# Performance work log

Hardware: AMD Instinct MI355X
Metric: run time of the kernel (lower is better)

The kernel has to match this reference:

```python
import jax, jax.numpy as jnp
import numpy as np

N, E, IN, H, O = 50000, 800000, 256, 8, 32


def setup_inputs() -> dict:
    key = jax.random.key(0)
    ks = jax.random.split(key, 8)
    feat = jax.random.normal(ks[0], (N, IN), dtype=jnp.float32)
    src = jax.random.randint(ks[1], (E,), 0, N, dtype=jnp.int32)
    dst = jax.random.randint(ks[2], (E,), 0, N, dtype=jnp.int32)
    # Xavier-normal-ish parameter init
    W = jax.random.normal(ks[3], (IN, H * O), dtype=jnp.float32) * (2.0 / (IN + H * O)) ** 0.5
    attn_l = jax.random.normal(ks[4], (H, O), dtype=jnp.float32) * (2.0 / (1 + H * O)) ** 0.5
    attn_r = jax.random.normal(ks[5], (H, O), dtype=jnp.float32) * (2.0 / (1 + H * O)) ** 0.5
    bias = jnp.zeros((H * O,), dtype=jnp.float32)
    return {"feat": feat, "W": W, "attn_l": attn_l, "attn_r": attn_r, "bias": bias, "src": src, "dst": dst}


def reference(feat, W, attn_l, attn_r, bias, src, dst):
    # Linear projection: [N, IN] @ [IN, H*O] -> [N, H, O]
    ft = (feat @ W).reshape(-1, H, O)
    # Additive attention logits per node, per head
    el = jnp.einsum('nho,ho->nh', ft, attn_l)  # [N, H]
    er = jnp.einsum('nho,ho->nh', ft, attn_r)  # [N, H]
    # Edge-wise: e = leaky_relu(el[u] + er[v])
    e = jax.nn.leaky_relu(el[src] + er[dst], negative_slope=0.2)  # [E, H]
    # Segment softmax over incoming edges of each destination node
    emax = jax.ops.segment_max(e, dst, num_segments=N)            # [N, H]
    ee = jnp.exp(e - emax[dst])                                   # [E, H]
    denom = jax.ops.segment_sum(ee, dst, num_segments=N)          # [N, H]
    a = ee / denom[dst]                                           # [E, H]
    # Weighted scatter-sum aggregation: sum_u a_{uv} * ft_u
    msg = ft[src] * a[:, :, None]                                 # [E, H, O]
    rst = jax.ops.segment_sum(msg, dst, num_segments=N)           # [N, H, O]
    rst = rst + bias.reshape(1, H, O)
    return rst
```

## Files before the change

### kernel.cpp

```cpp
#include <hip/hip_runtime.h>

#define N_NODES 50000
#define N_EDGES 800000
#define NPAD    50176
#define SPILL_CAP 8192
#define GEMM_BLOCKS 782
#define BUCKET_BLOCKS 1563

typedef __bf16 bf16x8 __attribute__((ext_vector_type(8)));
typedef float  fx4    __attribute__((ext_vector_type(4)));
typedef unsigned short us4 __attribute__((ext_vector_type(4)));
typedef unsigned short us8 __attribute__((ext_vector_type(8)));

__device__ __forceinline__ float b2f(unsigned short u) {
    return __uint_as_float(((unsigned)u) << 16);
}
__device__ __forceinline__ unsigned short f2b(float f) {
    unsigned x = __float_as_uint(f);
    return (unsigned short)((x + 0x7FFFu + ((x >> 16) & 1u)) >> 16);
}

__global__ __launch_bounds__(256) void prep_w(
    const float* __restrict__ W,
    const float* __restrict__ attn_l, const float* __restrict__ attn_r,
    unsigned short* __restrict__ Wt,
    unsigned short* __restrict__ M2t_hi, unsigned short* __restrict__ M2t_lo,
    int* __restrict__ cursor, int* __restrict__ spill_n) {
    int b = blockIdx.x, k = threadIdx.x;
    if (b < 256) {
        Wt[b * 256 + k] = f2b(W[k * 256 + b]);
    } else if (b < 272) {
        int j = b - 256;
        const float* av = (j < 8) ? (attn_l + j * 32) : (attn_r + (j - 8) * 32);
        int c0 = (j & 7) * 32;
        float s = 0.f;
#pragma unroll
        for (int o = 0; o < 32; ++o) s += W[k * 256 + c0 + o] * av[o];
        unsigned short h = f2b(s);
        M2t_hi[j * 256 + k] = h;
        M2t_lo[j * 256 + k] = f2b(s - b2f(h));
    } else {
        cursor[(b - 272) * 256 + k] = 0;
        if (b == 272 && k == 0) *spill_n = 0;
    }
}

__global__ __launch_bounds__(512) void gemm_bucket(
    const float* __restrict__ feat,
    const unsigned short* __restrict__ Wt,
    const unsigned short* __restrict__ M2t_hi,
    const unsigned short* __restrict__ M2t_lo,
    unsigned short* __restrict__ ft,
    float* __restrict__ el, float* __restrict__ er,
    const int* __restrict__ src, const int* __restrict__ dst,
    int* __restrict__ cursor, unsigned short* __restrict__ inedge,
    int* __restrict__ spill_n, int2* __restrict__ spill, int stride) {
    __shared__ unsigned short Alds[64 * 264];

    if (blockIdx.x >= GEMM_BLOCKS) {
        int t = (blockIdx.x - GEMM_BLOCKS) * 512 + threadIdx.x;
        if (t < N_EDGES) {
            int s = src[t], d = dst[t];
            int idx = atomicAdd(&cursor[d], 1);
            if (idx < stride) {
                inedge[(size_t)d * stride + idx] = (unsigned short)s;
            } else {
                int sp = atomicAdd(spill_n, 1);
                if (sp < SPILL_CAP) spill[sp] = make_int2(s, d);
            }
        }
        return;
    }

    const int tid  = threadIdx.x;
    const int lane = tid & 63;
    const int wid  = tid >> 6;
    const int quad = lane >> 4, l15 = lane & 15;
    const int mbase = blockIdx.x * 64;
    const int nbase = wid * 32;

    fx4 acc[4][2];
    fx4 acce[4];
#pragma unroll
    for (int i = 0; i < 4; ++i) {
        acce[i] = (fx4)0.0f;
#pragma unroll
        for (int j = 0; j < 2; ++j) acc[i][j] = (fx4)0.0f;
    }

    {
        const int srow = tid >> 3, s8 = tid & 7;
        int grow = mbase + srow;
        grow = grow < N_NODES ? grow : N_NODES - 1;
        const float* sp = feat + (size_t)grow * 256;
        unsigned short* sd = &Alds[srow * 264];
#pragma unroll
        for (int ii = 0; ii < 2; ++ii) {
            int c8 = ii * 16 + s8 * 2;
            float4 f0 = *reinterpret_cast<const float4*>(sp + c8 * 8);
            float4 f1 = *reinterpret_cast<const float4*>(sp + c8 * 8 + 4);
            float4 f2 = *reinterpret_cast<const float4*>(sp + c8 * 8 + 8);
            float4 f3 = *reinterpret_cast<const float4*>(sp + c8 * 8 + 12);
            us8 p0, p1;
            p0[0] = f2b(f0.x); p0[1] = f2b(f0.y); p0[2] = f2b(f0.z); p0[3] = f2b(f0.w);
            p0[4] = f2b(f1.x); p0[5] = f2b(f1.y); p0[6] = f2b(f1.z); p0[7] = f2b(f1.w);
            p1[0] = f2b(f2.x); p1[1] = f2b(f2.y); p1[2] = f2b(f2.z); p1[3] = f2b(f2.w);
            p1[4] = f2b(f3.x); p1[5] = f2b(f3.y); p1[6] = f2b(f3.z); p1[7] = f2b(f3.w);
            *reinterpret_cast<us8*>(sd + c8 * 8) = p0;
            *reinterpret_cast<us8*>(sd + c8 * 8 + 8) = p1;
        }
    }
    __syncthreads();

    for (int k0 = 0; k0 < 256; k0 += 32) {
        const int krow = k0 + quad * 8;
        bf16x8 a[4], b[2];
#pragma unroll
        for (int mt = 0; mt < 4; ++mt)
            a[mt] = *reinterpret_cast<const bf16x8*>(&Alds[(mt * 16 + l15) * 264 + krow]);
#pragma unroll
        for (int nt = 0; nt < 2; ++nt)
            b[nt] = *reinterpret_cast<const bf16x8*>(Wt + (nbase + nt * 16 + l15) * 256 + krow);
#pragma unroll
        for (int mt = 0; mt < 4; ++mt)
#pragma unroll
            for (int nt = 0; nt < 2; ++nt)
                acc[mt][nt] = __builtin_amdgcn_mfma_f32_16x16x32_bf16(
                    a[mt], b[nt], acc[mt][nt], 0, 0, 0);
        if (wid == 0) {
            bf16x8 bh = *reinterpret_cast<const bf16x8*>(M2t_hi + l15 * 256 + krow);
            bf16x8 bl = *reinterpret_cast<const bf16x8*>(M2t_lo + l15 * 256 + krow);
#pragma unroll
            for (int mt = 0; mt < 4; ++mt) {
                acce[mt] = __builtin_amdgcn_mfma_f32_16x16x32_bf16(a[mt], bh, acce[mt], 0, 0, 0);
                acce[mt] = __builtin_amdgcn_mfma_f32_16x16x32_bf16(a[mt], bl, acce[mt], 0, 0, 0);
            }
        }
    }
    __syncthreads();

    unsigned short* bw = &Alds[wid * 512];
#pragma unroll
    for (int mt = 0; mt < 4; ++mt) {
#pragma unroll
        for (int r = 0; r < 4; ++r) {
            int rl = quad * 4 + r;
#pragma unroll
            for (int nt = 0; nt < 2; ++nt)
                bw[rl * 32 + nt * 16 + l15] = f2b(acc[mt][nt][r]);
        }
        {
            int rl = lane >> 2;
            int c8 = lane & 3;
            us8 v = *reinterpret_cast<const us8*>(&bw[rl * 32 + c8 * 8]);
            int grow = mbase + mt * 16 + rl;
            if (grow < N_NODES)
                *reinterpret_cast<us8*>(ft + (size_t)grow * 256 + nbase + c8 * 8) = v;
        }
    }
    if (wid == 0) {
#pragma unroll
        for (int mt = 0; mt < 4; ++mt) {
#pragma unroll
            for (int r = 0; r < 4; ++r) {
                int row = mbase + mt * 16 + quad * 4 + r;
                if (row < N_NODES) {
                    float v = acce[mt][r];
                    if (l15 < 8) el[row * 8 + l15] = v;
                    else         er[row * 8 + (l15 - 8)] = v;
                }
            }
        }
    }
}

__global__ __launch_bounds__(128) void aggregate(
    const unsigned short* __restrict__ ft,
    const float* __restrict__ el, const float* __restrict__ er,
    const int* __restrict__ cursor,
    const unsigned short* __restrict__ inedge,
    const int* __restrict__ spill_n, const int2* __restrict__ spill,
    const float* __restrict__ bias,
    float* __restrict__ out, int stride) {
    int wid = threadIdx.x >> 6, lane = threadIdx.x & 63;
    int v = blockIdx.x * 2 + wid;
    int deg_t = cursor[v];
    int deg = deg_t < stride ? deg_t : stride;
    int half = lane >> 5, l = lane & 31;
    int h = l >> 2;
    float erv = er[v * 8 + h];
    const unsigned short* ip = inedge + (size_t)v * stride;
    const us8* ft8 = reinterpret_cast<const us8*>(ft);

    float a[8] = {0.f, 0.f, 0.f, 0.f, 0.f, 0.f, 0.f, 0.f};
    float s = 0.f;
    int j = 0;
    for (; j + 8 <= deg; j += 8) {
        int u[4];
#pragma unroll
        for (int t = 0; t < 4; ++t) u[t] = ip[j + 2 * t + half];
        us8 f[4];
#pragma unroll
        for (int t = 0; t < 4; ++t) f[t] = ft8[(size_t)u[t] * 32 + l];
#pragma unroll
        for (int t = 0; t < 4; ++t) {
            float x = el[u[t] * 8 + h] + erv;
            x = x > 0.f ? x : 0.2f * x;
            float w = __expf(x);
            s += w;
#pragma unroll
            for (int i = 0; i < 8; ++i) a[i] += w * b2f(f[t][i]);
        }
    }
    for (; j + 2 <= deg; j += 2) {
        int u = ip[j + half];
        us8 f = ft8[(size_t)u * 32 + l];
        float x = el[u * 8 + h] + erv;
        x = x > 0.f ? x : 0.2f * x;
        float w = __expf(x);
        s += w;
#pragma unroll
        for (int i = 0; i < 8; ++i) a[i] += w * b2f(f[i]);
    }
    if (j < deg && half == 0) {
        int u = ip[j];
        us8 f = ft8[(size_t)u * 32 + l];
        float x = el[u * 8 + h] + erv;
        x = x > 0.f ? x : 0.2f * x;
        float w = __expf(x);
        s += w;
#pragma unroll
        for (int i = 0; i < 8; ++i) a[i] += w * b2f(f[i]);
    }
    if (deg_t > stride) {
        int sn = *spill_n;
        if (sn > SPILL_CAP) sn = SPILL_CAP;
        for (int t = 0; t < sn; ++t) {
            int2 e = spill[t];
            if (e.y == v && half == 0) {
                int u = e.x;
                us8 f = ft8[(size_t)u * 32 + l];
                float x = el[u * 8 + h] + erv;
                x = x > 0.f ? x : 0.2f * x;
                float w = __expf(x);
                s += w;
#pragma unroll
                for (int i = 0; i < 8; ++i) a[i] += w * b2f(f[i]);
            }
        }
    }
#pragma unroll
    for (int i = 0; i < 8; ++i) a[i] += __shfl_xor(a[i], 32);
    s += __shfl_xor(s, 32);
    float inv = deg_t > 0 ? 1.0f / s : 0.f;

    int fi = l * 2 + half;
    float4 bb = reinterpret_cast<const float4*>(bias)[fi];
    int base = half * 4;
    float4 o;
    o.x = a[base + 0] * inv + bb.x;
    o.y = a[base + 1] * inv + bb.y;
    o.z = a[base + 2] * inv + bb.z;
    o.w = a[base + 3] * inv + bb.w;
    reinterpret_cast<float4*>(out)[(size_t)v * 64 + fi] = o;
}

extern "C" void kernel_launch(void* const* d_in, const int* in_sizes, int n_in,
                              void* d_out, int out_size, void* d_ws, size_t ws_size,
                              hipStream_t stream) {
    const float* feat   = (const float*)d_in[0];
    const float* W      = (const float*)d_in[1];
    const float* attn_l = (const float*)d_in[2];
    const float* attn_r = (const float*)d_in[3];
    const float* bias   = (const float*)d_in[4];
    const int* src = (const int*)d_in[5];
    const int* dst = (const int*)d_in[6];
    float* out = (float*)d_out;

    char* ws = (char*)d_ws;
    unsigned short* Wt     = (unsigned short*)(ws + 0);
    unsigned short* M2t_hi = (unsigned short*)(ws + 131072);
    unsigned short* M2t_lo = (unsigned short*)(ws + 139264);
    unsigned short* ft     = (unsigned short*)(ws + 147456);
    float* el              = (float*)(ws + 25747456);
    float* er              = (float*)(ws + 27347456);
    int* cursor            = (int*)(ws + 28947456);
    int* spill_n           = (int*)(ws + 29148160);
    int2* spill            = (int2*)(ws + 29148224);
    unsigned short* inedge = (unsigned short*)(ws + 29213760);

    size_t avail = ws_size > 29213760ull ? ws_size - 29213760ull : 0;
    int stride = (int)(avail / (2ull * NPAD));
    if (stride > 64) stride = 64;

    prep_w<<<468, 256, 0, stream>>>(W, attn_l, attn_r, Wt, M2t_hi, M2t_lo,
                                    cursor, spill_n);
    gemm_bucket<<<GEMM_BLOCKS + BUCKET_BLOCKS, 512, 0, stream>>>(
        feat, Wt, M2t_hi, M2t_lo, ft, el, er,
        src, dst, cursor, inedge, spill_n, spill, stride);
    aggregate<<<25000, 128, 0, stream>>>(ft, el, er, cursor, inedge,
                                         spill_n, spill, bias, out, stride);
}
```

Before: 225.9 us.

## Move attention logits to fp32 bucket blocks, prefetch W, vectorize edge loads

After: 316.4 us. +40.1%, slower.

```diff
diff --git a/kernel.cpp b/kernel.cpp
--- a/kernel.cpp
+++ b/kernel.cpp
@@ -9,7 +9,6 @@
 
 typedef __bf16 bf16x8 __attribute__((ext_vector_type(8)));
 typedef float  fx4    __attribute__((ext_vector_type(4)));
-typedef unsigned short us4 __attribute__((ext_vector_type(4)));
 typedef unsigned short us8 __attribute__((ext_vector_type(8)));
 
 __device__ __forceinline__ float b2f(unsigned short u) {
@@ -23,42 +22,55 @@
 __global__ __launch_bounds__(256) void prep_w(
     const float* __restrict__ W,
     const float* __restrict__ attn_l, const float* __restrict__ attn_r,
-    unsigned short* __restrict__ Wt,
-    unsigned short* __restrict__ M2t_hi, unsigned short* __restrict__ M2t_lo,
+    unsigned short* __restrict__ Wt, float* __restrict__ M2t,
     int* __restrict__ cursor, int* __restrict__ spill_n) {
-    int b = blockIdx.x, k = threadIdx.x;
-    if (b < 256) {
-        Wt[b * 256 + k] = f2b(W[k * 256 + b]);
-    } else if (b < 272) {
-        int j = b - 256;
+    __shared__ float T[64 * 65];
+    int b = blockIdx.x, t = threadIdx.x;
+    if (b < 16) {
+        int bi = b >> 2, bj = b & 3;
+        int r = t >> 2, cq = t & 3;
+        const float* wp = W + (size_t)(bi * 64 + r) * 256 + bj * 64 + cq * 16;
+#pragma unroll
+        for (int i = 0; i < 16; ++i) T[r * 65 + cq * 16 + i] = wp[i];
+        __syncthreads();
+        int n = t >> 2, ks = (t & 3) * 16;
+        us8 o0, o1;
+#pragma unroll
+        for (int i = 0; i < 8; ++i) o0[i] = f2b(T[(ks + i) * 65 + n]);
+#pragma unroll
+        for (int i = 0; i < 8; ++i) o1[i] = f2b(T[(ks + 8 + i) * 65 + n]);
+        unsigned short* op = Wt + (size_t)(bj * 64 + n) * 256 + bi * 64 + ks;
+        *reinterpret_cast<us8*>(op) = o0;
+        *reinterpret_cast<us8*>(op + 8) = o1;
+    } else if (b < 32) {
+        int j = b - 16;
         const float* av = (j < 8) ? (attn_l + j * 32) : (attn_r + (j - 8) * 32);
         int c0 = (j & 7) * 32;
         float s = 0.f;
 #pragma unroll
-        for (int o = 0; o < 32; ++o) s += W[k * 256 + c0 + o] * av[o];
-        unsigned short h = f2b(s);
-        M2t_hi[j * 256 + k] = h;
-        M2t_lo[j * 256 + k] = f2b(s - b2f(h));
+        for (int o = 0; o < 32; ++o) s += W[t * 256 + c0 + o] * av[o];
+        M2t[j * 256 + t] = s;
     } else {
-        cursor[(b - 272) * 256 + k] = 0;
-        if (b == 272 && k == 0) *spill_n = 0;
+        cursor[(b - 32) * 256 + t] = 0;
+        if (b == 32 && t == 0) *spill_n = 0;
     }
 }
 
 __global__ __launch_bounds__(512) void gemm_bucket(
     const float* __restrict__ feat,
     const unsigned short* __restrict__ Wt,
-    const unsigned short* __restrict__ M2t_hi,
-    const unsigned short* __restrict__ M2t_lo,
+    const float* __restrict__ M2t,
     unsigned short* __restrict__ ft,
     float* __restrict__ el, float* __restrict__ er,
     const int* __restrict__ src, const int* __restrict__ dst,
     int* __restrict__ cursor, unsigned short* __restrict__ inedge,
     int* __restrict__ spill_n, int2* __restrict__ spill, int stride) {
     __shared__ unsigned short Alds[64 * 264];
+    const int tid = threadIdx.x;
 
     if (blockIdx.x >= GEMM_BLOCKS) {
-        int t = (blockIdx.x - GEMM_BLOCKS) * 512 + threadIdx.x;
+        int bb = blockIdx.x - GEMM_BLOCKS;
+        int t = bb * 512 + tid;
         if (t < N_EDGES) {
             int s = src[t], d = dst[t];
             int idx = atomicAdd(&cursor[d], 1);
@@ -69,24 +81,62 @@
                 if (sp < SPILL_CAP) spill[sp] = make_int2(s, d);
             }
         }
+        if (bb < GEMM_BLOCKS) {
+            int row = bb * 64 + (tid >> 3);
+            int p = tid & 7;
+            if (row < N_NODES) {
+                const float4* fr = reinterpret_cast<const float4*>(
+                    feat + (size_t)row * 256 + p * 32);
+                float4 x[8];
+#pragma unroll
+                for (int i = 0; i < 8; ++i) x[i] = fr[i];
+                float pa[16];
+#pragma unroll
+                for (int jj = 0; jj < 16; ++jj) {
+                    const float4* mp = reinterpret_cast<const float4*>(
+                        M2t + jj * 256 + p * 32);
+                    float s = 0.f;
+#pragma unroll
+                    for (int i = 0; i < 8; ++i) {
+                        float4 m = mp[i];
+                        s += x[i].x * m.x + x[i].y * m.y +
+                             x[i].z * m.z + x[i].w * m.w;
+                    }
+                    pa[jj] = s;
+                }
+#pragma unroll
+                for (int jj = 0; jj < 16; ++jj) {
+                    pa[jj] += __shfl_xor(pa[jj], 1);
+                    pa[jj] += __shfl_xor(pa[jj], 2);
+                    pa[jj] += __shfl_xor(pa[jj], 4);
+                }
+                float outl = 0.f, outr = 0.f;
+#pragma unroll
+                for (int jj = 0; jj < 8; ++jj)
+                    if (p == jj) { outl = pa[jj]; outr = pa[8 + jj]; }
+                el[row * 8 + p] = outl;
+                er[row * 8 + p] = outr;
+            }
+        }
         return;
     }
 
-    const int tid  = threadIdx.x;
     const int lane = tid & 63;
     const int wid  = tid >> 6;
     const int quad = lane >> 4, l15 = lane & 15;
     const int mbase = blockIdx.x * 64;
     const int nbase = wid * 32;
 
+    const unsigned short* wb0 = Wt + (size_t)(nbase + l15) * 256 + quad * 8;
+    const unsigned short* wb1 = wb0 + 16 * 256;
+    bf16x8 bc0 = *reinterpret_cast<const bf16x8*>(wb0);
+    bf16x8 bc1 = *reinterpret_cast<const bf16x8*>(wb1);
+
     fx4 acc[4][2];
-    fx4 acce[4];
-#pragma unroll
-    for (int i = 0; i < 4; ++i) {
-        acce[i] = (fx4)0.0f;
+#pragma unroll
+    for (int i = 0; i < 4; ++i)
 #pragma unroll
         for (int j = 0; j < 2; ++j) acc[i][j] = (fx4)0.0f;
-    }
 
     {
         const int srow = tid >> 3, s8 = tid & 7;
@@ -113,29 +163,24 @@
     __syncthreads();
 
     for (int k0 = 0; k0 < 256; k0 += 32) {
+        bf16x8 bn0 = bc0, bn1 = bc1;
+        if (k0 < 224) {
+            bn0 = *reinterpret_cast<const bf16x8*>(wb0 + k0 + 32);
+            bn1 = *reinterpret_cast<const bf16x8*>(wb1 + k0 + 32);
+        }
         const int krow = k0 + quad * 8;
-        bf16x8 a[4], b[2];
+        bf16x8 a[4];
 #pragma unroll
         for (int mt = 0; mt < 4; ++mt)
             a[mt] = *reinterpret_cast<const bf16x8*>(&Alds[(mt * 16 + l15) * 264 + krow]);
-#pragma unroll
-        for (int nt = 0; nt < 2; ++nt)
-            b[nt] = *reinterpret_cast<const bf16x8*>(Wt + (nbase + nt * 16 + l15) * 256 + krow);
-#pragma unroll
-        for (int mt = 0; mt < 4; ++mt)
-#pragma unroll
-            for (int nt = 0; nt < 2; ++nt)
-                acc[mt][nt] = __builtin_amdgcn_mfma_f32_16x16x32_bf16(
-                    a[mt], b[nt], acc[mt][nt], 0, 0, 0);
-        if (wid == 0) {
-            bf16x8 bh = *reinterpret_cast<const bf16x8*>(M2t_hi + l15 * 256 + krow);
-            bf16x8 bl = *reinterpret_cast<const bf16x8*>(M2t_lo + l15 * 256 + krow);
-#pragma unroll
-            for (int mt = 0; mt < 4; ++mt) {
-                acce[mt] = __builtin_amdgcn_mfma_f32_16x16x32_bf16(a[mt], bh, acce[mt], 0, 0, 0);
-                acce[mt] = __builtin_amdgcn_mfma_f32_16x16x32_bf16(a[mt], bl, acce[mt], 0, 0, 0);
-            }
-        }
+        __builtin_amdgcn_s_setprio(1);
+#pragma unroll
+        for (int mt = 0; mt < 4; ++mt) {
+            acc[mt][0] = __builtin_amdgcn_mfma_f32_16x16x32_bf16(a[mt], bc0, acc[mt][0], 0, 0, 0);
+            acc[mt][1] = __builtin_amdgcn_mfma_f32_16x16x32_bf16(a[mt], bc1, acc[mt][1], 0, 0, 0);
+        }
+        __builtin_amdgcn_s_setprio(0);
+        bc0 = bn0; bc1 = bn1;
     }
     __syncthreads();
 
@@ -156,20 +201,6 @@
             int grow = mbase + mt * 16 + rl;
             if (grow < N_NODES)
                 *reinterpret_cast<us8*>(ft + (size_t)grow * 256 + nbase + c8 * 8) = v;
-        }
-    }
-    if (wid == 0) {
-#pragma unroll
-        for (int mt = 0; mt < 4; ++mt) {
-#pragma unroll
-            for (int r = 0; r < 4; ++r) {
-                int row = mbase + mt * 16 + quad * 4 + r;
-                if (row < N_NODES) {
-                    float v = acce[mt][r];
-                    if (l15 < 8) el[row * 8 + l15] = v;
-                    else         er[row * 8 + (l15 - 8)] = v;
-                }
-            }
         }
     }
 }
@@ -188,6 +219,7 @@
     int deg = deg_t < stride ? deg_t : stride;
     int half = lane >> 5, l = lane & 31;
     int h = l >> 2;
+    int sh = half * 16;
     float erv = er[v * 8 + h];
     const unsigned short* ip = inedge + (size_t)v * stride;
     const us8* ft8 = reinterpret_cast<const us8*>(ft);
@@ -195,10 +227,35 @@
     float a[8] = {0.f, 0.f, 0.f, 0.f, 0.f, 0.f, 0.f, 0.f};
     float s = 0.f;
     int j = 0;
+    for (; j + 16 <= deg; j += 16) {
+        uint4 q0 = *reinterpret_cast<const uint4*>(ip + j);
+        uint4 q1 = *reinterpret_cast<const uint4*>(ip + j + 8);
+        int u[8];
+        u[0] = (q0.x >> sh) & 0xffff; u[1] = (q0.y >> sh) & 0xffff;
+        u[2] = (q0.z >> sh) & 0xffff; u[3] = (q0.w >> sh) & 0xffff;
+        u[4] = (q1.x >> sh) & 0xffff; u[5] = (q1.y >> sh) & 0xffff;
+        u[6] = (q1.z >> sh) & 0xffff; u[7] = (q1.w >> sh) & 0xffff;
+        us8 f[8];
+#pragma unroll
+        for (int t = 0; t < 8; ++t) f[t] = ft8[(size_t)u[t] * 32 + l];
+        float ee[8];
+#pragma unroll
+        for (int t = 0; t < 8; ++t) ee[t] = el[u[t] * 8 + h];
+#pragma unroll
+        for (int t = 0; t < 8; ++t) {
+            float x = ee[t] + erv;
+            x = x > 0.f ? x : 0.2f * x;
+            float w = __expf(x);
+            s += w;
+#pragma unroll
+            for (int i = 0; i < 8; ++i) a[i] += w * b2f(f[t][i]);
+        }
+    }
     for (; j + 8 <= deg; j += 8) {
+        uint4 q0 = *reinterpret_cast<const uint4*>(ip + j);
         int u[4];
-#pragma unroll
-        for (int t = 0; t < 4; ++t) u[t] = ip[j + 2 * t + half];
+        u[0] = (q0.x >> sh) & 0xffff; u[1] = (q0.y >> sh) & 0xffff;
+        u[2] = (q0.z >> sh) & 0xffff; u[3] = (q0.w >> sh) & 0xffff;
         us8 f[4];
 #pragma unroll
         for (int t = 0; t < 4; ++t) f[t] = ft8[(size_t)u[t] * 32 + l];
@@ -279,8 +336,7 @@
 
     char* ws = (char*)d_ws;
     unsigned short* Wt     = (unsigned short*)(ws + 0);
-    unsigned short* M2t_hi = (unsigned short*)(ws + 131072);
-    unsigned short* M2t_lo = (unsigned short*)(ws + 139264);
+    float* M2t             = (float*)(ws + 131072);
     unsigned short* ft     = (unsigned short*)(ws + 147456);
     float* el              = (float*)(ws + 25747456);
     float* er              = (float*)(ws + 27347456);
@@ -291,12 +347,14 @@
 
     size_t avail = ws_size > 29213760ull ? ws_size - 29213760ull : 0;
     int stride = (int)(avail / (2ull * NPAD));
+    stride &= ~7;
     if (stride > 64) stride = 64;
-
-    prep_w<<<468, 256, 0, stream>>>(W, attn_l, attn_r, Wt, M2t_hi, M2t_lo,
+    if (stride < 8) stride = 8;
+
+    prep_w<<<228, 256, 0, stream>>>(W, attn_l, attn_r, Wt, M2t,
                                     cursor, spill_n);
     gemm_bucket<<<GEMM_BLOCKS + BUCKET_BLOCKS, 512, 0, stream>>>(
-        feat, Wt, M2t_hi, M2t_lo, ft, el, er,
+        feat, Wt, M2t, ft, el, er,
         src, dst, cursor, inedge, spill_n, spill, stride);
     aggregate<<<25000, 128, 0, stream>>>(ft, el, er, cursor, inedge,
                                          spill_n, spill, bias, out, stride);
```

## Compute attention logits in GEMM epilogue, swizzle LDS, tile W transpose

Applied to the files above, without the earlier changes.

After: 236.5 us. 4.7% more time.

```diff
diff --git a/kernel.cpp b/kernel.cpp
--- a/kernel.cpp
+++ b/kernel.cpp
@@ -9,7 +9,6 @@
 
 typedef __bf16 bf16x8 __attribute__((ext_vector_type(8)));
 typedef float  fx4    __attribute__((ext_vector_type(4)));
-typedef unsigned short us4 __attribute__((ext_vector_type(4)));
 typedef unsigned short us8 __attribute__((ext_vector_type(8)));
 
 __device__ __forceinline__ float b2f(unsigned short u) {
@@ -22,43 +21,47 @@
 
 __global__ __launch_bounds__(256) void prep_w(
     const float* __restrict__ W,
-    const float* __restrict__ attn_l, const float* __restrict__ attn_r,
     unsigned short* __restrict__ Wt,
-    unsigned short* __restrict__ M2t_hi, unsigned short* __restrict__ M2t_lo,
     int* __restrict__ cursor, int* __restrict__ spill_n) {
-    int b = blockIdx.x, k = threadIdx.x;
-    if (b < 256) {
-        Wt[b * 256 + k] = f2b(W[k * 256 + b]);
-    } else if (b < 272) {
-        int j = b - 256;
-        const float* av = (j < 8) ? (attn_l + j * 32) : (attn_r + (j - 8) * 32);
-        int c0 = (j & 7) * 32;
-        float s = 0.f;
-#pragma unroll
-        for (int o = 0; o < 32; ++o) s += W[k * 256 + c0 + o] * av[o];
-        unsigned short h = f2b(s);
-        M2t_hi[j * 256 + k] = h;
-        M2t_lo[j * 256 + k] = f2b(s - b2f(h));
+    __shared__ float T[64 * 65];
+    int b = blockIdx.x, t = threadIdx.x;
+    if (b < 16) {
+        int bi = b >> 2, bj = b & 3;
+        int r = t >> 2, cq = t & 3;
+        const float* wp = W + (size_t)(bi * 64 + r) * 256 + bj * 64 + cq * 16;
+#pragma unroll
+        for (int i = 0; i < 16; ++i) T[r * 65 + cq * 16 + i] = wp[i];
+        __syncthreads();
+        int n = t >> 2, ks = (t & 3) * 16;
+        us8 o0, o1;
+#pragma unroll
+        for (int i = 0; i < 8; ++i) o0[i] = f2b(T[(ks + i) * 65 + n]);
+#pragma unroll
+        for (int i = 0; i < 8; ++i) o1[i] = f2b(T[(ks + 8 + i) * 65 + n]);
+        unsigned short* op = Wt + (size_t)(bj * 64 + n) * 256 + bi * 64 + ks;
+        *reinterpret_cast<us8*>(op) = o0;
+        *reinterpret_cast<us8*>(op + 8) = o1;
     } else {
-        cursor[(b - 272) * 256 + k] = 0;
-        if (b == 272 && k == 0) *spill_n = 0;
+        cursor[(b - 16) * 256 + t] = 0;
+        if (b == 16 && t == 0) *spill_n = 0;
     }
 }
 
 __global__ __launch_bounds__(512) void gemm_bucket(
     const float* __restrict__ feat,
     const unsigned short* __restrict__ Wt,
-    const unsigned short* __restrict__ M2t_hi,
-    const unsigned short* __restrict__ M2t_lo,
+    const float* __restrict__ attn_l, const float* __restrict__ attn_r,
     unsigned short* __restrict__ ft,
     float* __restrict__ el, float* __restrict__ er,
     const int* __restrict__ src, const int* __restrict__ dst,
     int* __restrict__ cursor, unsigned short* __restrict__ inedge,
     int* __restrict__ spill_n, int2* __restrict__ spill, int stride) {
-    __shared__ unsigned short Alds[64 * 264];
+    __shared__ unsigned short Alds[64 * 256];
+    __shared__ float elds[2][64][8];
+    const int tid = threadIdx.x;
 
     if (blockIdx.x >= GEMM_BLOCKS) {
-        int t = (blockIdx.x - GEMM_BLOCKS) * 512 + threadIdx.x;
+        int t = (blockIdx.x - GEMM_BLOCKS) * 512 + tid;
         if (t < N_EDGES) {
             int s = src[t], d = dst[t];
             int idx = atomicAdd(&cursor[d], 1);
@@ -72,105 +75,109 @@
         return;
     }
 
-    const int tid  = threadIdx.x;
     const int lane = tid & 63;
     const int wid  = tid >> 6;
     const int quad = lane >> 4, l15 = lane & 15;
     const int mbase = blockIdx.x * 64;
     const int nbase = wid * 32;
 
+    const unsigned short* wb0 = Wt + (size_t)(nbase + l15) * 256 + quad * 8;
+    const unsigned short* wb1 = wb0 + 16 * 256;
+    bf16x8 bc0 = *reinterpret_cast<const bf16x8*>(wb0);
+    bf16x8 bc1 = *reinterpret_cast<const bf16x8*>(wb1);
+
+    float al0 = attn_l[nbase + l15], al1 = attn_l[nbase + 16 + l15];
+    float ar0 = attn_r[nbase + l15], ar1 = attn_r[nbase + 16 + l15];
+
     fx4 acc[4][2];
-    fx4 acce[4];
-#pragma unroll
-    for (int i = 0; i < 4; ++i) {
-        acce[i] = (fx4)0.0f;
+#pragma unroll
+    for (int i = 0; i < 4; ++i)
 #pragma unroll
         for (int j = 0; j < 2; ++j) acc[i][j] = (fx4)0.0f;
-    }
 
     {
         const int srow = tid >> 3, s8 = tid & 7;
         int grow = mbase + srow;
         grow = grow < N_NODES ? grow : N_NODES - 1;
         const float* sp = feat + (size_t)grow * 256;
-        unsigned short* sd = &Alds[srow * 264];
-#pragma unroll
-        for (int ii = 0; ii < 2; ++ii) {
-            int c8 = ii * 16 + s8 * 2;
-            float4 f0 = *reinterpret_cast<const float4*>(sp + c8 * 8);
-            float4 f1 = *reinterpret_cast<const float4*>(sp + c8 * 8 + 4);
-            float4 f2 = *reinterpret_cast<const float4*>(sp + c8 * 8 + 8);
-            float4 f3 = *reinterpret_cast<const float4*>(sp + c8 * 8 + 12);
-            us8 p0, p1;
-            p0[0] = f2b(f0.x); p0[1] = f2b(f0.y); p0[2] = f2b(f0.z); p0[3] = f2b(f0.w);
-            p0[4] = f2b(f1.x); p0[5] = f2b(f1.y); p0[6] = f2b(f1.z); p0[7] = f2b(f1.w);
-            p1[0] = f2b(f2.x); p1[1] = f2b(f2.y); p1[2] = f2b(f2.z); p1[3] = f2b(f2.w);
-            p1[4] = f2b(f3.x); p1[5] = f2b(f3.y); p1[6] = f2b(f3.z); p1[7] = f2b(f3.w);
-            *reinterpret_cast<us8*>(sd + c8 * 8) = p0;
-            *reinterpret_cast<us8*>(sd + c8 * 8 + 8) = p1;
+        unsigned short* sd = Alds + srow * 256;
+        const int r7 = srow & 7;
+#pragma unroll
+        for (int ii = 0; ii < 4; ++ii) {
+            int c16 = ii * 8 + s8;
+            float4 f0 = *reinterpret_cast<const float4*>(sp + c16 * 8);
+            float4 f1 = *reinterpret_cast<const float4*>(sp + c16 * 8 + 4);
+            us8 p;
+            p[0] = f2b(f0.x); p[1] = f2b(f0.y); p[2] = f2b(f0.z); p[3] = f2b(f0.w);
+            p[4] = f2b(f1.x); p[5] = f2b(f1.y); p[6] = f2b(f1.z); p[7] = f2b(f1.w);
+            *reinterpret_cast<us8*>(sd + (c16 ^ r7) * 8) = p;
         }
     }
     __syncthreads();
 
     for (int k0 = 0; k0 < 256; k0 += 32) {
-        const int krow = k0 + quad * 8;
-        bf16x8 a[4], b[2];
-#pragma unroll
-        for (int mt = 0; mt < 4; ++mt)
-            a[mt] = *reinterpret_cast<const bf16x8*>(&Alds[(mt * 16 + l15) * 264 + krow]);
-#pragma unroll
-        for (int nt = 0; nt < 2; ++nt)
-            b[nt] = *reinterpret_cast<const bf16x8*>(Wt + (nbase + nt * 16 + l15) * 256 + krow);
-#pragma unroll
-        for (int mt = 0; mt < 4; ++mt)
-#pragma unroll
-            for (int nt = 0; nt < 2; ++nt)
-                acc[mt][nt] = __builtin_amdgcn_mfma_f32_16x16x32_bf16(
-                    a[mt], b[nt], acc[mt][nt], 0, 0, 0);
-        if (wid == 0) {
-            bf16x8 bh = *reinterpret_cast<const bf16x8*>(M2t_hi + l15 * 256 + krow);
-            bf16x8 bl = *reinterpret_cast<const bf16x8*>(M2t_lo + l15 * 256 + krow);
-#pragma unroll
-            for (int mt = 0; mt < 4; ++mt) {
-                acce[mt] = __builtin_amdgcn_mfma_f32_16x16x32_bf16(a[mt], bh, acce[mt], 0, 0, 0);
-                acce[mt] = __builtin_amdgcn_mfma_f32_16x16x32_bf16(a[mt], bl, acce[mt], 0, 0, 0);
+        bf16x8 bn0 = bc0, bn1 = bc1;
+        if (k0 < 224) {
+            bn0 = *reinterpret_cast<const bf16x8*>(wb0 + k0 + 32);
+            bn1 = *reinterpret_cast<const bf16x8*>(wb1 + k0 + 32);
+        }
+        const int c16 = (k0 >> 3) + quad;
+        bf16x8 a[4];
+#pragma unroll
+        for (int mt = 0; mt < 4; ++mt) {
+            int row = mt * 16 + l15;
+            a[mt] = *reinterpret_cast<const bf16x8*>(
+                Alds + row * 256 + ((c16 ^ (row & 7)) * 8));
+        }
+#pragma unroll
+        for (int mt = 0; mt < 4; ++mt) {
+            acc[mt][0] = __builtin_amdgcn_mfma_f32_16x16x32_bf16(a[mt], bc0, acc[mt][0], 0, 0, 0);
+            acc[mt][1] = __builtin_amdgcn_mfma_f32_16x16x32_bf16(a[mt], bc1, acc[mt][1], 0, 0, 0);
+        }
+        bc0 = bn0; bc1 = bn1;
+    }
+    __syncthreads();
+
+#pragma unroll
+    for (int mt = 0; mt < 4; ++mt) {
+#pragma unroll
+        for (int r = 0; r < 4; ++r) {
+            int row = mt * 16 + quad * 4 + r;
+            int r7 = row & 7;
+#pragma unroll
+            for (int nt = 0; nt < 2; ++nt) {
+                int c16 = (nbase >> 3) + nt * 2 + (l15 >> 3);
+                Alds[row * 256 + ((c16 ^ r7) * 8) + (l15 & 7)] = f2b(acc[mt][nt][r]);
             }
+            float cl = acc[mt][0][r] * al0 + acc[mt][1][r] * al1;
+            float cr = acc[mt][0][r] * ar0 + acc[mt][1][r] * ar1;
+#pragma unroll
+            for (int m = 1; m < 16; m <<= 1) {
+                cl += __shfl_xor(cl, m);
+                cr += __shfl_xor(cr, m);
+            }
+            if (l15 == 0)      elds[0][row][wid] = cl;
+            else if (l15 == 1) elds[1][row][wid] = cr;
         }
     }
     __syncthreads();
 
-    unsigned short* bw = &Alds[wid * 512];
-#pragma unroll
-    for (int mt = 0; mt < 4; ++mt) {
-#pragma unroll
-        for (int r = 0; r < 4; ++r) {
-            int rl = quad * 4 + r;
-#pragma unroll
-            for (int nt = 0; nt < 2; ++nt)
-                bw[rl * 32 + nt * 16 + l15] = f2b(acc[mt][nt][r]);
-        }
-        {
-            int rl = lane >> 2;
-            int c8 = lane & 3;
-            us8 v = *reinterpret_cast<const us8*>(&bw[rl * 32 + c8 * 8]);
-            int grow = mbase + mt * 16 + rl;
-            if (grow < N_NODES)
-                *reinterpret_cast<us8*>(ft + (size_t)grow * 256 + nbase + c8 * 8) = v;
-        }
-    }
-    if (wid == 0) {
-#pragma unroll
-        for (int mt = 0; mt < 4; ++mt) {
-#pragma unroll
-            for (int r = 0; r < 4; ++r) {
-                int row = mbase + mt * 16 + quad * 4 + r;
-                if (row < N_NODES) {
-                    float v = acce[mt][r];
-                    if (l15 < 8) el[row * 8 + l15] = v;
-                    else         er[row * 8 + (l15 - 8)] = v;
-                }
-            }
-        }
+#pragma unroll
+    for (int i = 0; i < 4; ++i) {
+        int g = i * 512 + tid;
+        int row = g >> 5, c16 = g & 31;
+        us8 v = *reinterpret_cast<const us8*>(
+            Alds + row * 256 + ((c16 ^ (row & 7)) * 8));
+        if (mbase + row < N_NODES)
+            *reinterpret_cast<us8*>(ft + (size_t)(mbase + row) * 256 + c16 * 8) = v;
+    }
+    if (tid < 256) {
+        int sel = tid >> 7, t = tid & 127;
+        int row = t >> 1;
+        float4 v = *reinterpret_cast<const float4*>(&elds[sel][0][0] + t * 4);
+        float* dstp = sel ? er : el;
+        if (mbase + row < N_NODES)
+            *reinterpret_cast<float4*>(dstp + (size_t)(mbase + row) * 8 + (t & 1) * 4) = v;
     }
 }
 
@@ -279,8 +286,6 @@
 
     char* ws = (char*)d_ws;
     unsigned short* Wt     = (unsigned short*)(ws + 0);
-    unsigned short* M2t_hi = (unsigned short*)(ws + 131072);
-    unsigned short* M2t_lo = (unsigned short*)(ws + 139264);
     unsigned short* ft     = (unsigned short*)(ws + 147456);
     float* el              = (float*)(ws + 25747456);
     float* er              = (float*)(ws + 27347456);
@@ -293,10 +298,9 @@
     int stride = (int)(avail / (2ull * NPAD));
     if (stride > 64) stride = 64;
 
-    prep_w<<<468, 256, 0, stream>>>(W, attn_l, attn_r, Wt, M2t_hi, M2t_lo,
-                                    cursor, spill_n);
+    prep_w<<<212, 256, 0, stream>>>(W, Wt, cursor, spill_n);
     gemm_bucket<<<GEMM_BLOCKS + BUCKET_BLOCKS, 512, 0, stream>>>(
-        feat, Wt, M2t_hi, M2t_lo, ft, el, er,
+        feat, Wt, attn_l, attn_r, ft, el, er,
         src, dst, cursor, inedge, spill_n, spill, stride);
     aggregate<<<25000, 128, 0, stream>>>(ft, el, er, cursor, inedge,
                                          spill_n, spill, bias, out, stride);
```
